# Kernel optimization log

Measured on AMD Instinct MI355X. Metric: run time of the kernel, lower is better.

The kernel has to match this reference:

```python
import jax, jax.numpy as jnp
import numpy as np

B, N, C, K, T = 64, 1024, 256, 512, 64
D_THRESH = 0.5
POWER_ITERS = 20


def _pdist(x):
    # x: [..., K, 3] -> pairwise euclidean distances [..., K, K]
    n = jnp.sum(x * x, axis=-1)
    sq = n[..., :, None] + n[..., None, :] - 2.0 * jnp.einsum('...kc,...lc->...kl', x, x)
    return jnp.sqrt(jnp.maximum(sq, 0.0) + 1e-12)


def _forward(rt, rt_centroids, rt_cls_attn, shift_and_scale, W_in, b_in, W1, b1, W2, b2,
             num_rt, anc_idx, pos_idx, neg_idx):
    valid = jnp.arange(N)[None, :] < num_rt[:, None]                      # [B,N]
    # Normalize.batch_unnormalize: pts * scale + shift on valid tokens
    shift = shift_and_scale[:, None, :3]
    scale = shift_and_scale[:, None, 3:4]
    cent = jnp.where(valid[..., None], rt_centroids * scale + shift, rt_centroids)
    attn = jnp.where(valid, rt_cls_attn, -1e9)
    _, top_idx = jax.lax.top_k(attn, K)                                   # [B,K]
    cent_k = jnp.take_along_axis(cent, top_idx[..., None], axis=1)        # [B,K,3]
    rt_k = jnp.take_along_axis(rt, top_idx[..., None], axis=1)            # [B,K,C]
    # SGV padding mask [T,2,K,K]: rows masked by anchor count, cols by pos/neg counts
    n_eff = jnp.minimum(num_rt, K)
    r = jnp.arange(K)
    row_mask = r[None, :] < n_eff[anc_idx][:, None]                       # [T,K]
    col_mask = jnp.stack([r[None, :] < n_eff[pos_idx][:, None],
                          r[None, :] < n_eff[neg_idx][:, None]], axis=1)  # [T,2,K]
    mask = row_mask[:, None, :, None] & col_mask[:, :, None, :]           # [T,2,K,K]
    # input_linear on anchor / neighbour relay tokens
    anc_f = rt_k[anc_idx] @ W_in + b_in                                   # [T,K,C]
    nn_f = jnp.stack([rt_k[pos_idx], rt_k[neg_idx]], axis=1) @ W_in + b_in  # [T,2,K,C]
    anc_c = cent_k[anc_idx]                                               # [T,K,3]
    nn_c = jnp.stack([cent_k[pos_idx], cent_k[neg_idx]], axis=1)          # [T,2,K,3]
    # feature-space nearest-neighbour correspondences anc -> nn (SpectralGV style)
    fd = (jnp.sum(anc_f ** 2, -1)[:, None, :, None]
          + jnp.sum(nn_f ** 2, -1)[:, :, None, :]
          - 2.0 * jnp.einsum('tkc,tnlc->tnkl', anc_f, nn_f))              # [T,2,K,K]
    corr = jnp.argmin(fd, axis=-1)                                        # [T,2,K]
    q_c = jnp.take_along_axis(nn_c, corr[..., None], axis=2)              # [T,2,K,3]
    q_f = jnp.take_along_axis(nn_f, corr[..., None], axis=2)              # [T,2,K,C]
    # correspondence confidence from feature cosine similarity
    cos = jnp.sum(anc_f[:, None] * q_f, -1) / (
        jnp.linalg.norm(anc_f, axis=-1)[:, None] * jnp.linalg.norm(q_f, axis=-1) + 1e-8)
    s = jax.nn.relu(cos)                                                  # [T,2,K]
    # threshold-masked geometric consistency adjacency
    d_p = _pdist(anc_c)[:, None]                                          # [T,1,K,K]
    d_q = _pdist(q_c)                                                     # [T,2,K,K]
    geo = (jnp.abs(d_p - d_q) < D_THRESH) & mask & (~jnp.eye(K, dtype=bool))
    A = geo.astype(jnp.float32) * s[..., :, None] * s[..., None, :]       # [T,2,K,K]
    # leading eigenvector via power iteration (A is entrywise nonnegative)
    v = jnp.full((T, 2, K), 1.0 / np.sqrt(K), dtype=jnp.float32)
    for _ in range(POWER_ITERS):
        w = jnp.einsum('tnkl,tnl->tnk', A, v)
        v = w / (jnp.linalg.norm(w, axis=-1, keepdims=True) + 1e-8)
    eig = -jnp.sort(-v, axis=-1)                                          # sort_eigvec, descending
    h = jax.nn.relu(eig @ W1 + b1)
    scores = jax.nn.sigmoid(h @ W2 + b2)                                  # [T,2,1]
    targets = jnp.zeros_like(scores).at[:, 0].set(1.0)
    return scores, targets


def setup_inputs() -> dict:
    key = jax.random.key(0)
    ks = jax.random.split(key, 12)
    return {
        'rt': jax.random.normal(ks[0], (B, N, C), jnp.float32),
        'rt_centroids': jax.random.normal(ks[1], (B, N, 3), jnp.float32),
        'rt_cls_attn': jax.random.uniform(ks[2], (B, N), jnp.float32),
        'shift_and_scale': jax.random.uniform(ks[3], (B, 4), jnp.float32),
        'num_rt': jax.random.randint(ks[4], (B,), 128, N, jnp.int32),
        'anc_idx': jax.random.randint(ks[5], (T,), 0, B, jnp.int32),
        'pos_idx': jax.random.randint(ks[6], (T,), 0, B, jnp.int32),
        'neg_idx': jax.random.randint(ks[7], (T,), 0, B, jnp.int32),
        'W_in': jax.random.normal(ks[8], (C, C), jnp.float32) / np.sqrt(C),
        'b_in': jnp.zeros((C,), jnp.float32),
        'W1': jax.random.normal(ks[9], (K, K), jnp.float32) / np.sqrt(K),
        'b1': jnp.zeros((K,), jnp.float32),
        'W2': jax.random.normal(ks[10], (K, 1), jnp.float32) / np.sqrt(K),
        'b2': jnp.zeros((1,), jnp.float32),
    }


def reference(rt, rt_centroids, rt_cls_attn, shift_and_scale, num_rt, anc_idx, pos_idx, neg_idx,
              W_in, b_in, W1, b1, W2, b2):
    return _forward(rt, rt_centroids, rt_cls_attn, shift_and_scale, W_in, b_in, W1, b1, W2, b2,
                    num_rt, anc_idx, pos_idx, neg_idx)
```

## Files before the change

### kernel.cpp

```cpp
#include <hip/hip_runtime.h>
#include <cstddef>

#define BB 64
#define NN 1024
#define CC 256
#define KK 512
#define TT 64
#define NPAIR 128

typedef _Float16 h8 __attribute__((ext_vector_type(8)));
typedef _Float16 h4 __attribute__((ext_vector_type(4)));
typedef float f4 __attribute__((ext_vector_type(4)));

typedef __attribute__((address_space(1))) const void GV;
typedef __attribute__((address_space(3))) void LV;
#define GLDS16(g, s) __builtin_amdgcn_global_load_lds((GV*)(const void*)(g), (LV*)(void*)(s), 16, 0, 0)


__global__ __launch_bounds__(256) void wtrans_kernel(
    const float* __restrict__ Win, _Float16* __restrict__ wth, _Float16* __restrict__ wtl)
{
    __shared__ float t[64][65];
    const int k0 = blockIdx.x * 64, n0 = blockIdx.y * 64;
    const int tid = threadIdx.x;
    const int c = tid & 63, r0 = tid >> 6;
    for (int r = r0; r < 64; r += 4)
        t[r][c] = Win[(size_t)(k0 + r) * CC + n0 + c];
    __syncthreads();
    for (int r = r0; r < 64; r += 4) {
        float x = t[c][r];
        _Float16 h = (_Float16)x;
        size_t o = (size_t)(n0 + r) * CC + k0 + c;
        wth[o] = h;
        wtl[o] = (_Float16)(x - (float)h);
    }
}

__global__ __launch_bounds__(512) void sel_kernel(
    const float* __restrict__ attn, const float* __restrict__ cents,
    const float* __restrict__ sas, const int* __restrict__ num_rt,
    int* __restrict__ topidx, int* __restrict__ neff, float* __restrict__ centk)
{
    __shared__ unsigned long long keys[1024];
    const int b = blockIdx.x, tid = threadIdx.x;
    const int nr = num_rt[b];
    for (int i = tid; i < 1024; i += 512) {
        float a = (i < nr) ? attn[b * NN + i] : -1e9f;
        unsigned u = __float_as_uint(a);
        u = (u & 0x80000000u) ? ~u : (u | 0x80000000u);
        keys[i] = ((unsigned long long)u << 32) | (unsigned)(0xFFFFFFFFu - (unsigned)i);
    }
    __syncthreads();
    for (int k = 2; k <= 1024; k <<= 1) {
        for (int j = k >> 1; j > 0; j >>= 1) {
            int i = ((tid & ~(j - 1)) << 1) | (tid & (j - 1));
            int p = i | j;
            unsigned long long a = keys[i], c = keys[p];
            bool up = (i & k) == 0;
            if (up ? (a < c) : (a > c)) { keys[i] = c; keys[p] = a; }
            __syncthreads();
        }
    }
    {
        unsigned long long key = keys[tid];
        int idx = (int)(~(unsigned)key);
        float x = cents[(b * NN + idx) * 3 + 0];
        float y = cents[(b * NN + idx) * 3 + 1];
        float z = cents[(b * NN + idx) * 3 + 2];
        if (idx < nr) {
            float sc = sas[b * 4 + 3];
            x = x * sc + sas[b * 4 + 0];
            y = y * sc + sas[b * 4 + 1];
            z = z * sc + sas[b * 4 + 2];
        }
        float nc = x * x + y * y + z * z;
        ((float4*)centk)[b * KK + tid] = make_float4(x, y, z, nc);
        topidx[b * KK + tid] = idx;
    }
    if (tid == 0) neff[b] = (nr < KK) ? nr : KK;
}

__global__ __launch_bounds__(256) void feat_mfma(
    const float* __restrict__ rt, const int* __restrict__ topidx,
    const _Float16* __restrict__ wth, const _Float16* __restrict__ wtl,
    const float* __restrict__ bin,
    _Float16* __restrict__ feath, _Float16* __restrict__ featl)
{
    const int mtile = blockIdx.x, nt = blockIdx.y;
    __shared__ _Float16 Ah[128][32], Al[128][32], Bh[128][32], Bl[128][32];
    __shared__ int tix[128];
    const int tid = threadIdx.x;
    const int w = tid >> 6, lane = tid & 63;
    const int quad = lane >> 4, l16 = lane & 15;
    const int wm = (w >> 1) * 64, wl = (w & 1) * 64;
    const int b = mtile >> 2;
    if (tid < 128) tix[tid] = topidx[mtile * 128 + tid];
    __syncthreads();
    const float* arow = (tid < 128) ? rt + ((size_t)b * NN + tix[tid]) * CC : rt;
    const _Float16* bplane = (w == 2) ? wth : wtl;
    _Float16* bsh = (w == 2) ? &Bh[0][0] : &Bl[0][0];
    const int rowi = lane >> 2, chunk = lane & 3;

    f4 acc[4][4];
    #pragma unroll
    for (int i = 0; i < 4; i++)
        #pragma unroll
        for (int j = 0; j < 4; j++)
            acc[i][j] = (f4){0.f, 0.f, 0.f, 0.f};

    for (int k0 = 0; k0 < CC; k0 += 32) {
        __syncthreads();
        if (w < 2) {
            const float4* src = (const float4*)(arow + k0);
            #pragma unroll
            for (int c = 0; c < 4; c++) {
                float4 p = src[2 * c], q2 = src[2 * c + 1];
                float xv[8] = {p.x, p.y, p.z, p.w, q2.x, q2.y, q2.z, q2.w};
                h8 hv, lv;
                #pragma unroll
                for (int j = 0; j < 8; j++) {
                    _Float16 h = (_Float16)xv[j];
                    hv[j] = h;
                    lv[j] = (_Float16)(xv[j] - (float)h);
                }
                *(h8*)&Ah[tid][c * 8] = hv;
                *(h8*)&Al[tid][c * 8] = lv;
            }
        } else {
            #pragma unroll
            for (int j = 0; j < 8; j++) {
                int row = j * 16 + rowi;
                const _Float16* ga = bplane + (size_t)(nt * 128 + row) * CC + k0 + chunk * 8;
                GLDS16(ga, bsh + j * 512);
            }
        }
        __syncthreads();
        h8 afh[4], afl[4], bfh[4], bfl[4];
        #pragma unroll
        for (int i = 0; i < 4; i++) {
            int ra = wm + i * 16 + l16;
            int rb = wl + i * 16 + l16;
            afh[i] = *(const h8*)&Ah[ra][quad * 8];
            afl[i] = *(const h8*)&Al[ra][quad * 8];
            bfh[i] = *(const h8*)&Bh[rb][quad * 8];
            bfl[i] = *(const h8*)&Bl[rb][quad * 8];
        }
        #pragma unroll
        for (int i = 0; i < 4; i++)
            #pragma unroll
            for (int j = 0; j < 4; j++) {
                acc[i][j] = __builtin_amdgcn_mfma_f32_16x16x32_f16(afh[i], bfh[j], acc[i][j], 0, 0, 0);
                acc[i][j] = __builtin_amdgcn_mfma_f32_16x16x32_f16(afh[i], bfl[j], acc[i][j], 0, 0, 0);
                acc[i][j] = __builtin_amdgcn_mfma_f32_16x16x32_f16(afl[i], bfh[j], acc[i][j], 0, 0, 0);
            }
    }
    #pragma unroll
    for (int j = 0; j < 4; j++) {
        int col = wl + j * 16 + l16;
        float bj = bin[nt * 128 + col];
        #pragma unroll
        for (int i = 0; i < 4; i++)
            #pragma unroll
            for (int r = 0; r < 4; r++) {
                int row = wm + i * 16 + quad * 4 + r;
                float v = acc[i][j][r] + bj;
                _Float16 h = (_Float16)v;
                size_t o = (size_t)(mtile * 128 + row) * CC + nt * 128 + col;
                feath[o] = h;
                featl[o] = (_Float16)(v - (float)h);
            }
    }
}

__global__ __launch_bounds__(256) void norm_kernel(
    const _Float16* __restrict__ feath, const _Float16* __restrict__ featl,
    float* __restrict__ normF)
{
    int r = blockIdx.x * 4 + (threadIdx.x >> 6);
    int lane = threadIdx.x & 63;
    h4 hv = ((const h4*)(feath + (size_t)r * CC))[lane];
    h4 lv = ((const h4*)(featl + (size_t)r * CC))[lane];
    float s = 0.f;
    #pragma unroll
    for (int j = 0; j < 4; j++) {
        float x = (float)hv[j] + (float)lv[j];
        s += x * x;
    }
    for (int off = 32; off; off >>= 1) s += __shfl_down(s, off);
    if (lane == 0) normF[r] = s;
}

__global__ __launch_bounds__(256) void argmin_mfma(
    const _Float16* __restrict__ feath, const _Float16* __restrict__ featl,
    const float* __restrict__ normF,
    const int* __restrict__ anc, const int* __restrict__ pos, const int* __restrict__ neg,
    float* __restrict__ partv, int* __restrict__ partl, float* __restrict__ partd)
{
    const int lt = blockIdx.x, kt = blockIdx.y, pr = blockIdx.z;
    const int t = pr >> 1, nn2 = pr & 1;
    const int a = anc[t];
    const int bb = nn2 ? neg[t] : pos[t];
    const size_t Abase = ((size_t)a * KK + kt * 128) * CC;
    const size_t Bbase = ((size_t)bb * KK + lt * 128) * CC;
    __shared__ _Float16 Ah[128][32], Al[128][32], Bh[128][32], Bl[128][32];
    __shared__ float rdv[128][2];
    __shared__ int   rdl[128][2];
    __shared__ float rdd[128][2];
    const int tid = threadIdx.x;
    const int w = tid >> 6, lane = tid & 63;
    const int quad = lane >> 4, l16 = lane & 15;
    const int wm = (w >> 1) * 64, wl = (w & 1) * 64;
    const int rowi = lane >> 2, chunk = lane & 3;
    const _Float16* gplane = (w == 0) ? feath + Abase : (w == 1) ? featl + Abase
                           : (w == 2) ? feath + Bbase : featl + Bbase;
    _Float16* splane = (w == 0) ? &Ah[0][0] : (w == 1) ? &Al[0][0]
                     : (w == 2) ? &Bh[0][0] : &Bl[0][0];
    const _Float16* grow = gplane + (size_t)rowi * CC + chunk * 8;

    f4 acc[4][4];
    #pragma unroll
    for (int i = 0; i < 4; i++)
        #pragma unroll
        for (int j = 0; j < 4; j++)
            acc[i][j] = (f4){0.f, 0.f, 0.f, 0.f};

    for (int k0 = 0; k0 < CC; k0 += 32) {
        __syncthreads();
        #pragma unroll
        for (int j = 0; j < 8; j++)
            GLDS16(grow + (size_t)(j * 16) * CC + k0, splane + j * 512);
        __syncthreads();
        h8 afh[4], afl[4], bfh[4], bfl[4];
        #pragma unroll
        for (int i = 0; i < 4; i++) {
            int ra = wm + i * 16 + l16;
            int rb = wl + i * 16 + l16;
            afh[i] = *(const h8*)&Ah[ra][quad * 8];
            afl[i] = *(const h8*)&Al[ra][quad * 8];
            bfh[i] = *(const h8*)&Bh[rb][quad * 8];
            bfl[i] = *(const h8*)&Bl[rb][quad * 8];
        }
        #pragma unroll
        for (int i = 0; i < 4; i++)
            #pragma unroll
            for (int j = 0; j < 4; j++) {
                acc[i][j] = __builtin_amdgcn_mfma_f32_16x16x32_f16(afh[i], bfh[j], acc[i][j], 0, 0, 0);
                acc[i][j] = __builtin_amdgcn_mfma_f32_16x16x32_f16(afh[i], bfl[j], acc[i][j], 0, 0, 0);
                acc[i][j] = __builtin_amdgcn_mfma_f32_16x16x32_f16(afl[i], bfh[j], acc[i][j], 0, 0, 0);
            }
    }
    float nbj[4];
    #pragma unroll
    for (int j = 0; j < 4; j++)
        nbj[j] = normF[(size_t)bb * KK + lt * 128 + wl + j * 16 + l16];
    #pragma unroll
    for (int i = 0; i < 4; i++) {
        #pragma unroll
        for (int r = 0; r < 4; r++) {
            float bv = INFINITY; int bl = 0; float bd = 0.f;
            #pragma unroll
            for (int j = 0; j < 4; j++) {
                float d = acc[i][j][r];
                float v = nbj[j] - 2.f * d;
                int l = lt * 128 + wl + j * 16 + l16;
                if (v < bv) { bv = v; bl = l; bd = d; }
            }
            #pragma unroll
            for (int off = 1; off < 16; off <<= 1) {
                float ov = __shfl_xor(bv, off);
                int   ol = __shfl_xor(bl, off);
                float od = __shfl_xor(bd, off);
                if (ov < bv || (ov == bv && ol < bl)) { bv = ov; bl = ol; bd = od; }
            }
            if (l16 == 0) {
                int row = wm + i * 16 + quad * 4 + r;
                rdv[row][w & 1] = bv;
                rdl[row][w & 1] = bl;
                rdd[row][w & 1] = bd;
            }
        }
    }
    __syncthreads();
    if (tid < 128) {
        float bv = rdv[tid][0]; int bl = rdl[tid][0]; float bd = rdd[tid][0];
        float v1 = rdv[tid][1]; int l1 = rdl[tid][1];
        if (v1 < bv || (v1 == bv && l1 < bl)) { bv = v1; bl = l1; bd = rdd[tid][1]; }
        size_t idx = (((size_t)pr * 4 + kt) * 128 + tid) * 4 + lt;
        partv[idx] = bv; partl[idx] = bl; partd[idx] = bd;
    }
}

__global__ __launch_bounds__(256) void argmin_fin(
    const float* __restrict__ partv, const int* __restrict__ partl,
    const float* __restrict__ partd, const float* __restrict__ normF,
    const int* __restrict__ anc, const int* __restrict__ pos, const int* __restrict__ neg,
    int* __restrict__ corr, float* __restrict__ sbuf)
{
    int g = blockIdx.x * 256 + threadIdx.x;
    int pr = g >> 9, kg = g & 511;
    int t = pr >> 1, nn2 = pr & 1;
    int a = anc[t];
    int bb = nn2 ? neg[t] : pos[t];
    size_t base = (size_t)g * 4;
    float bv = partv[base]; int bl = partl[base]; float bd = partd[base];
    #pragma unroll
    for (int lt = 1; lt < 4; lt++) {
        float v = partv[base + lt]; int l = partl[base + lt];
        if (v < bv || (v == bv && l < bl)) { bv = v; bl = l; bd = partd[base + lt]; }
    }
    float na = normF[(size_t)a * KK + kg];
    float nb = normF[(size_t)bb * KK + bl];
    float cosv = bd / (sqrtf(na) * sqrtf(nb) + 1e-8f);
    corr[g] = bl;
    sbuf[g] = fmaxf(cosv, 0.f);
}

__global__ __launch_bounds__(256) void geo_kernel(
    const float* __restrict__ centk, const int* __restrict__ corr,
    const int* __restrict__ neff,
    const int* __restrict__ anc, const int* __restrict__ pos, const int* __restrict__ neg,
    unsigned* __restrict__ gmask)
{
    const int kt = blockIdx.x;
    const int lt = blockIdx.y;
    const int pair = blockIdx.z;
    const int t = pair >> 1, nn2 = pair & 1;
    const int a = anc[t];
    const int bb2 = (nn2 == 0) ? pos[t] : neg[t];
    const int nea = neff[a], neb = neff[bb2];
    __shared__ __align__(16) float4 ca[512], cq[512];
    for (int i = threadIdx.x; i < KK; i += 256) {
        ca[i] = ((const float4*)centk)[a * KK + i];
        int c = corr[pair * KK + i];
        cq[i] = ((const float4*)centk)[bb2 * KK + c];
    }
    __syncthreads();
    const int k = kt * 256 + threadIdx.x;
    float4 pk = ca[k], qk = cq[k];
    bool rowm = k < nea;
    unsigned* outp = gmask + ((size_t)pair * KK + k) * 16 + lt * 4;
    for (int w = 0; w < 4; w++) {
        unsigned word = 0;
        #pragma unroll
        for (int bi = 0; bi < 32; bi++) {
            int l = lt * 128 + w * 32 + bi;
            float4 pl = ca[l], ql = cq[l];
            float dp2 = pk.w + pl.w - 2.f * (pk.x * pl.x + pk.y * pl.y + pk.z * pl.z);
            float dp = sqrtf(fmaxf(dp2, 0.f) + 1e-12f);
            float dq2 = qk.w + ql.w - 2.f * (qk.x * ql.x + qk.y * ql.y + qk.z * ql.z);
            float dq = sqrtf(fmaxf(dq2, 0.f) + 1e-12f);
            bool g = (fabsf(dp - dq) < 0.5f) && rowm && (l < neb) && (l != k);
            word |= (g ? (1u << bi) : 0u);
        }
        outp[w] = word;
    }
}

__global__ __launch_bounds__(1024, 4) void power_kernel(
    const unsigned* __restrict__ gmask, const float* __restrict__ sbuf,
    const float* __restrict__ W1, const float* __restrict__ b1,
    const float* __restrict__ W2, const float* __restrict__ b2,
    float* __restrict__ out)
{
    const int pair = blockIdx.x;
    const int tid = threadIdx.x;
    const int row = tid & 511;
    const int half = tid >> 9;
    __shared__ __align__(16) float u[512];
    __shared__ float T[64][257];
    __shared__ float pacc[1024];
    __shared__ float red[16];
    __shared__ float ev[512];
    __shared__ float hpart[1024];
    unsigned m[8];
    const unsigned* g = gmask + ((size_t)pair * KK + row) * 16 + half * 8;
    #pragma unroll
    for (int w = 0; w < 8; w++) m[w] = g[w];
    const float s = sbuf[pair * KK + row];
    const int bp = tid & 63;
    const int vh = tid >> 6;
    const int GV_[16] = {0,1,3,2,6,7,5,4,12,13,15,14,10,11,9,8};
    const int GB[15] = {0,1,0,2,0,1,0,3,0,1,0,2,0,1,0};
    const float GS[15] = {1.f,1.f,-1.f,1.f,1.f,-1.f,-1.f,1.f,1.f,1.f,-1.f,-1.f,1.f,-1.f,-1.f};
    float v = 0.044194173824159216f;
    if (half == 0) u[row] = s * v;
    __syncthreads();
    for (int it = 0; it < 20; it++) {
        {
            float4 ulo = *(const float4*)&u[bp * 8];
            float4 uhi = *(const float4*)&u[bp * 8 + 4];
            float ul[4] = {ulo.x, ulo.y, ulo.z, ulo.w};
            float H = 0.f;
            H += (float)((vh >> 0) & 1) * uhi.x;
            H += (float)((vh >> 1) & 1) * uhi.y;
            H += (float)((vh >> 2) & 1) * uhi.z;
            H += (float)((vh >> 3) & 1) * uhi.w;
            float L = 0.f;
            T[bp][vh * 16 + 0] = H;
            #pragma unroll
            for (int k = 1; k < 16; k++) {
                L += GS[k - 1] * ul[GB[k - 1]];
                T[bp][vh * 16 + GV_[k]] = H + L;
            }
        }
        __syncthreads();
        float a0 = 0.f, a1 = 0.f, a2 = 0.f, a3 = 0.f;
        #pragma unroll
        for (int w = 0; w < 8; w++) {
            unsigned mw = m[w];
            const int p0 = half * 32 + w * 4;
            a0 += T[p0 + 0][mw & 255u];
            a1 += T[p0 + 1][(mw >> 8) & 255u];
            a2 += T[p0 + 2][(mw >> 16) & 255u];
            a3 += T[p0 + 3][mw >> 24];
        }
        pacc[tid] = (a0 + a1) + (a2 + a3);
        __syncthreads();
        float wk = s * (pacc[row] + pacc[row + 512]);
        float t2 = wk * wk;
        for (int off = 32; off; off >>= 1) t2 += __shfl_down(t2, off);
        if ((tid & 63) == 0) red[tid >> 6] = t2;
        __syncthreads();
        float tot = 0.f;
        #pragma unroll
        for (int x = 0; x < 16; x++) tot += red[x];
        tot *= 0.5f;
        v = wk / (sqrtf(tot) + 1e-8f);
        if (half == 0) u[row] = s * v;
        __syncthreads();
    }
    if (half == 0) ev[row] = v;
    __syncthreads();
    for (int kk = 2; kk <= 512; kk <<= 1) {
        for (int j = kk >> 1; j; j >>= 1) {
            if (tid < 256) {
                int i = ((tid & ~(j - 1)) << 1) | (tid & (j - 1));
                int p = i | j;
                float x = ev[i], y = ev[p];
                bool up = (i & kk) == 0;
                if (up ? (x < y) : (x > y)) { ev[i] = y; ev[p] = x; }
            }
            __syncthreads();
        }
    }
    const int cbase = half * 256;
    float h = (half == 0) ? b1[row] : 0.f;
    #pragma unroll 8
    for (int l = 0; l < 256; l++)
        h += ev[cbase + l] * W1[(size_t)(cbase + l) * KK + row];
    hpart[tid] = h;
    __syncthreads();
    float term = 0.f;
    if (half == 0) {
        float hv = fmaxf(hpart[row] + hpart[row + 512], 0.f);
        term = hv * W2[row];
    }
    for (int off = 32; off; off >>= 1) term += __shfl_down(term, off);
    if ((tid & 63) == 0) red[tid >> 6] = term;
    __syncthreads();
    if (tid == 0) {
        float sc = 0.f;
        #pragma unroll
        for (int x = 0; x < 16; x++) sc += red[x];
        sc += b2[0];
        out[pair] = 1.f / (1.f + expf(-sc));
        out[NPAIR + pair] = (pair & 1) ? 0.f : 1.f;
    }
}

extern "C" void kernel_launch(void* const* d_in, const int* in_sizes, int n_in,
                              void* d_out, int out_size, void* d_ws, size_t ws_size,
                              hipStream_t stream) {
    (void)in_sizes; (void)n_in; (void)out_size; (void)ws_size;
    const float* rt    = (const float*)d_in[0];
    const float* cents = (const float*)d_in[1];
    const float* attn  = (const float*)d_in[2];
    const float* sas   = (const float*)d_in[3];
    const int* num_rt  = (const int*)d_in[4];
    const int* anc     = (const int*)d_in[5];
    const int* pos     = (const int*)d_in[6];
    const int* neg     = (const int*)d_in[7];
    const float* Win   = (const float*)d_in[8];
    const float* bin   = (const float*)d_in[9];
    const float* W1    = (const float*)d_in[10];
    const float* b1    = (const float*)d_in[11];
    const float* W2    = (const float*)d_in[12];
    const float* b2    = (const float*)d_in[13];

    float* ws = (float*)d_ws;
    _Float16* feath = (_Float16*)ws;
    _Float16* featl = (_Float16*)(ws + 4194304);
    float* normF = ws + 8388608;
    float* centk = ws + 8421376;
    float* sbuf  = ws + 8552448;
    int* topidx  = (int*)(ws + 8617984);
    int* neffp   = (int*)(ws + 8650752);
    int* corr    = (int*)(ws + 8650816);
    unsigned* gmask = (unsigned*)(ws + 8716352);
    float* partv = (float*)(ws + 8716352);
    int*   partl = (int*)(ws + 8716352 + 262144);
    float* partd = (float*)(ws + 8716352 + 524288);
    _Float16* wth = (_Float16*)(ws + 8716352 + 786432);
    _Float16* wtl = (_Float16*)(ws + 8716352 + 819200);
    float* out = (float*)d_out;

    wtrans_kernel<<<dim3(4, 4), 256, 0, stream>>>(Win, wth, wtl);
    sel_kernel<<<64, 512, 0, stream>>>(attn, cents, sas, num_rt, topidx, neffp, centk);
    feat_mfma<<<dim3(256, 2), 256, 0, stream>>>(rt, topidx, wth, wtl, bin, feath, featl);
    norm_kernel<<<8192, 256, 0, stream>>>(feath, featl, normF);
    argmin_mfma<<<dim3(4, 4, 128), 256, 0, stream>>>(feath, featl, normF, anc, pos, neg, partv, partl, partd);
    argmin_fin<<<256, 256, 0, stream>>>(partv, partl, partd, normF, anc, pos, neg, corr, sbuf);
    geo_kernel<<<dim3(2, 4, 128), 256, 0, stream>>>(centk, corr, neffp, anc, pos, neg, gmask);
    power_kernel<<<128, 1024, 0, stream>>>(gmask, sbuf, W1, b1, W2, b2, out);
}
```

Before: 376.5 us.

## Share anchor tile across pos and neg pairs in argmin MFMA kernel

Each argmin block now handles both the positive and negative neighbour for a triplet, using 512 threads. The anchor hi/lo tiles are loaded into shared memory once and reused by both halves, so anchor global loads drop by about half and the grid shrinks from 2048 to 1024 blocks. In exchange each block uses more LDS and more threads, which may reduce occupancy, and two waves sit idle during loads.

```diff
diff --git a/kernel.cpp b/kernel.cpp
--- a/kernel.cpp
+++ b/kernel.cpp
@@ -190,32 +190,38 @@
     if (lane == 0) normF[r] = s;
 }
 
-__global__ __launch_bounds__(256) void argmin_mfma(
+__global__ __launch_bounds__(512) void argmin_mfma(
     const _Float16* __restrict__ feath, const _Float16* __restrict__ featl,
     const float* __restrict__ normF,
     const int* __restrict__ anc, const int* __restrict__ pos, const int* __restrict__ neg,
     float* __restrict__ partv, int* __restrict__ partl, float* __restrict__ partd)
 {
-    const int lt = blockIdx.x, kt = blockIdx.y, pr = blockIdx.z;
-    const int t = pr >> 1, nn2 = pr & 1;
-    const int a = anc[t];
-    const int bb = nn2 ? neg[t] : pos[t];
+    const int lt = blockIdx.x, kt = blockIdx.y, t = blockIdx.z;
+    const int a = anc[t], bp = pos[t], bn = neg[t];
     const size_t Abase = ((size_t)a * KK + kt * 128) * CC;
-    const size_t Bbase = ((size_t)bb * KK + lt * 128) * CC;
-    __shared__ _Float16 Ah[128][32], Al[128][32], Bh[128][32], Bl[128][32];
-    __shared__ float rdv[128][2];
-    __shared__ int   rdl[128][2];
-    __shared__ float rdd[128][2];
+    const size_t Pbase = ((size_t)bp * KK + lt * 128) * CC;
+    const size_t Nbase = ((size_t)bn * KK + lt * 128) * CC;
+    __shared__ _Float16 smem[6 * 4096];
+    __shared__ float rdv[2][128][2];
+    __shared__ int   rdl[2][128][2];
+    __shared__ float rdd[2][128][2];
     const int tid = threadIdx.x;
     const int w = tid >> 6, lane = tid & 63;
     const int quad = lane >> 4, l16 = lane & 15;
-    const int wm = (w >> 1) * 64, wl = (w & 1) * 64;
+    const int pair = w & 1, wmI = (w >> 1) & 1, wlI = (w >> 2) & 1;
+    const int wm = wmI * 64, wl = wlI * 64;
     const int rowi = lane >> 2, chunk = lane & 3;
-    const _Float16* gplane = (w == 0) ? feath + Abase : (w == 1) ? featl + Abase
-                           : (w == 2) ? feath + Bbase : featl + Bbase;
-    _Float16* splane = (w == 0) ? &Ah[0][0] : (w == 1) ? &Al[0][0]
-                     : (w == 2) ? &Bh[0][0] : &Bl[0][0];
+    const _Float16* gplane =
+        (w == 0) ? feath + Abase : (w == 1) ? featl + Abase :
+        (w == 2) ? feath + Pbase : (w == 3) ? featl + Pbase :
+        (w == 4) ? feath + Nbase : featl + Nbase;
+    _Float16* splane = smem + (w < 6 ? w : 0) * 4096;
     const _Float16* grow = gplane + (size_t)rowi * CC + chunk * 8;
+    const _Float16* Ah = smem;
+    const _Float16* Al = smem + 4096;
+    const _Float16* Bhp = smem + (pair ? 4 : 2) * 4096;
+    const _Float16* Blp = smem + (pair ? 5 : 3) * 4096;
+    const int bb = pair ? bn : bp;
 
     f4 acc[4][4];
     #pragma unroll
@@ -226,19 +232,21 @@
 
     for (int k0 = 0; k0 < CC; k0 += 32) {
         __syncthreads();
-        #pragma unroll
-        for (int j = 0; j < 8; j++)
-            GLDS16(grow + (size_t)(j * 16) * CC + k0, splane + j * 512);
+        if (w < 6) {
+            #pragma unroll
+            for (int j = 0; j < 8; j++)
+                GLDS16(grow + (size_t)(j * 16) * CC + k0, splane + j * 512);
+        }
         __syncthreads();
         h8 afh[4], afl[4], bfh[4], bfl[4];
         #pragma unroll
         for (int i = 0; i < 4; i++) {
             int ra = wm + i * 16 + l16;
             int rb = wl + i * 16 + l16;
-            afh[i] = *(const h8*)&Ah[ra][quad * 8];
-            afl[i] = *(const h8*)&Al[ra][quad * 8];
-            bfh[i] = *(const h8*)&Bh[rb][quad * 8];
-            bfl[i] = *(const h8*)&Bl[rb][quad * 8];
+            afh[i] = *(const h8*)&Ah[ra * 32 + quad * 8];
+            afl[i] = *(const h8*)&Al[ra * 32 + quad * 8];
+            bfh[i] = *(const h8*)&Bhp[rb * 32 + quad * 8];
+            bfl[i] = *(const h8*)&Blp[rb * 32 + quad * 8];
         }
         #pragma unroll
         for (int i = 0; i < 4; i++)
@@ -274,18 +282,20 @@
             }
             if (l16 == 0) {
                 int row = wm + i * 16 + quad * 4 + r;
-                rdv[row][w & 1] = bv;
-                rdl[row][w & 1] = bl;
-                rdd[row][w & 1] = bd;
-            }
-        }
-    }
-    __syncthreads();
-    if (tid < 128) {
-        float bv = rdv[tid][0]; int bl = rdl[tid][0]; float bd = rdd[tid][0];
-        float v1 = rdv[tid][1]; int l1 = rdl[tid][1];
-        if (v1 < bv || (v1 == bv && l1 < bl)) { bv = v1; bl = l1; bd = rdd[tid][1]; }
-        size_t idx = (((size_t)pr * 4 + kt) * 128 + tid) * 4 + lt;
+                rdv[pair][row][wlI] = bv;
+                rdl[pair][row][wlI] = bl;
+                rdd[pair][row][wlI] = bd;
+            }
+        }
+    }
+    __syncthreads();
+    if (tid < 256) {
+        const int pairIdx = tid >> 7, row = tid & 127;
+        float bv = rdv[pairIdx][row][0]; int bl = rdl[pairIdx][row][0]; float bd = rdd[pairIdx][row][0];
+        float v1 = rdv[pairIdx][row][1]; int l1 = rdl[pairIdx][row][1];
+        if (v1 < bv || (v1 == bv && l1 < bl)) { bv = v1; bl = l1; bd = rdd[pairIdx][row][1]; }
+        int pr = t * 2 + pairIdx;
+        size_t idx = (((size_t)pr * 4 + kt) * 128 + row) * 4 + lt;
         partv[idx] = bv; partl[idx] = bl; partd[idx] = bd;
     }
 }
@@ -508,7 +518,7 @@
     sel_kernel<<<64, 512, 0, stream>>>(attn, cents, sas, num_rt, topidx, neffp, centk);
     feat_mfma<<<dim3(256, 2), 256, 0, stream>>>(rt, topidx, wth, wtl, bin, feath, featl);
     norm_kernel<<<8192, 256, 0, stream>>>(feath, featl, normF);
-    argmin_mfma<<<dim3(4, 4, 128), 256, 0, stream>>>(feath, featl, normF, anc, pos, neg, partv, partl, partd);
+    argmin_mfma<<<dim3(4, 4, 64), 512, 0, stream>>>(feath, featl, normF, anc, pos, neg, partv, partl, partd);
     argmin_fin<<<256, 256, 0, stream>>>(partv, partl, partd, normF, anc, pos, neg, corr, sbuf);
     geo_kernel<<<dim3(2, 4, 128), 256, 0, stream>>>(centk, corr, neffp, anc, pos, neg, gmask);
     power_kernel<<<128, 1024, 0, stream>>>(gmask, sbuf, W1, b1, W2, b2, out);
```

Result: slower. 386.5 us (+2.7%).

## Fuse argmin finalization into geo kernel and rebalance feat_mfma load roles

Applied to the files above, without the earlier changes.

The separate argmin_fin launch is removed. Each geo_kernel block now reduces the four partial argmin candidates itself to get the correspondence indices, and only one block per pair writes the cosine scores. This saves a launch and the corr round trip through global memory, but every one of the 8 blocks per pair repeats the small reduction. Separately, feat_mfma now has all four waves share the A-row fp32-to-fp16 split (two threads per row) and the B-tile async LDS loads, instead of splitting waves between the two tasks. The partial buffers are moved so they no longer alias gmask, since both are now live in the same kernel.

```diff
diff --git a/kernel.cpp b/kernel.cpp
--- a/kernel.cpp
+++ b/kernel.cpp
@@ -96,9 +96,11 @@
     const int b = mtile >> 2;
     if (tid < 128) tix[tid] = topidx[mtile * 128 + tid];
     __syncthreads();
-    const float* arow = (tid < 128) ? rt + ((size_t)b * NN + tix[tid]) * CC : rt;
-    const _Float16* bplane = (w == 2) ? wth : wtl;
-    _Float16* bsh = (w == 2) ? &Bh[0][0] : &Bl[0][0];
+    const int arow_i = tid >> 1;
+    const int aseg = (tid & 1) * 16;
+    const float* arow = rt + ((size_t)b * NN + tix[arow_i]) * CC + aseg;
+    _Float16* bsh = (w < 2) ? &Bh[0][0] : &Bl[0][0];
+    const _Float16* bplane = (w < 2) ? wth : wtl;
     const int rowi = lane >> 2, chunk = lane & 3;
 
     f4 acc[4][4];
@@ -110,10 +112,16 @@
 
     for (int k0 = 0; k0 < CC; k0 += 32) {
         __syncthreads();
-        if (w < 2) {
+        #pragma unroll
+        for (int jj = 0; jj < 4; jj++) {
+            int j = (w & 1) * 4 + jj;
+            int row = j * 16 + rowi;
+            GLDS16(bplane + (size_t)(nt * 128 + row) * CC + k0 + chunk * 8, bsh + j * 512);
+        }
+        {
             const float4* src = (const float4*)(arow + k0);
             #pragma unroll
-            for (int c = 0; c < 4; c++) {
+            for (int c = 0; c < 2; c++) {
                 float4 p = src[2 * c], q2 = src[2 * c + 1];
                 float xv[8] = {p.x, p.y, p.z, p.w, q2.x, q2.y, q2.z, q2.w};
                 h8 hv, lv;
@@ -123,15 +131,8 @@
                     hv[j] = h;
                     lv[j] = (_Float16)(xv[j] - (float)h);
                 }
-                *(h8*)&Ah[tid][c * 8] = hv;
-                *(h8*)&Al[tid][c * 8] = lv;
-            }
-        } else {
-            #pragma unroll
-            for (int j = 0; j < 8; j++) {
-                int row = j * 16 + rowi;
-                const _Float16* ga = bplane + (size_t)(nt * 128 + row) * CC + k0 + chunk * 8;
-                GLDS16(ga, bsh + j * 512);
+                *(h8*)&Ah[arow_i][aseg + c * 8] = hv;
+                *(h8*)&Al[arow_i][aseg + c * 8] = lv;
             }
         }
         __syncthreads();
@@ -290,60 +291,55 @@
     }
 }
 
-__global__ __launch_bounds__(256) void argmin_fin(
+__global__ __launch_bounds__(256) void geo_kernel(
+    const float* __restrict__ centk,
     const float* __restrict__ partv, const int* __restrict__ partl,
     const float* __restrict__ partd, const float* __restrict__ normF,
-    const int* __restrict__ anc, const int* __restrict__ pos, const int* __restrict__ neg,
-    int* __restrict__ corr, float* __restrict__ sbuf)
-{
-    int g = blockIdx.x * 256 + threadIdx.x;
-    int pr = g >> 9, kg = g & 511;
-    int t = pr >> 1, nn2 = pr & 1;
-    int a = anc[t];
-    int bb = nn2 ? neg[t] : pos[t];
-    size_t base = (size_t)g * 4;
-    float bv = partv[base]; int bl = partl[base]; float bd = partd[base];
-    #pragma unroll
-    for (int lt = 1; lt < 4; lt++) {
-        float v = partv[base + lt]; int l = partl[base + lt];
-        if (v < bv || (v == bv && l < bl)) { bv = v; bl = l; bd = partd[base + lt]; }
-    }
-    float na = normF[(size_t)a * KK + kg];
-    float nb = normF[(size_t)bb * KK + bl];
-    float cosv = bd / (sqrtf(na) * sqrtf(nb) + 1e-8f);
-    corr[g] = bl;
-    sbuf[g] = fmaxf(cosv, 0.f);
-}
-
-__global__ __launch_bounds__(256) void geo_kernel(
-    const float* __restrict__ centk, const int* __restrict__ corr,
     const int* __restrict__ neff,
     const int* __restrict__ anc, const int* __restrict__ pos, const int* __restrict__ neg,
-    unsigned* __restrict__ gmask)
+    float* __restrict__ sbuf, unsigned* __restrict__ gmask)
 {
     const int kt = blockIdx.x;
-    const int lt = blockIdx.y;
+    const int lt4 = blockIdx.y;
     const int pair = blockIdx.z;
     const int t = pair >> 1, nn2 = pair & 1;
     const int a = anc[t];
     const int bb2 = (nn2 == 0) ? pos[t] : neg[t];
     const int nea = neff[a], neb = neff[bb2];
+    const bool writer = (kt == 0) && (lt4 == 0);
+    __shared__ int ci[512];
     __shared__ __align__(16) float4 ca[512], cq[512];
     for (int i = threadIdx.x; i < KK; i += 256) {
+        size_t base = ((size_t)pair * KK + i) * 4;
+        float bv = partv[base]; int bl = partl[base]; float bd = partd[base];
+        #pragma unroll
+        for (int lt = 1; lt < 4; lt++) {
+            float v = partv[base + lt]; int l = partl[base + lt];
+            if (v < bv || (v == bv && l < bl)) { bv = v; bl = l; bd = partd[base + lt]; }
+        }
+        ci[i] = bl;
+        if (writer) {
+            float na = normF[(size_t)a * KK + i];
+            float nb = normF[(size_t)bb2 * KK + bl];
+            float cosv = bd / (sqrtf(na) * sqrtf(nb) + 1e-8f);
+            sbuf[pair * KK + i] = fmaxf(cosv, 0.f);
+        }
+    }
+    __syncthreads();
+    for (int i = threadIdx.x; i < KK; i += 256) {
         ca[i] = ((const float4*)centk)[a * KK + i];
-        int c = corr[pair * KK + i];
-        cq[i] = ((const float4*)centk)[bb2 * KK + c];
+        cq[i] = ((const float4*)centk)[bb2 * KK + ci[i]];
     }
     __syncthreads();
     const int k = kt * 256 + threadIdx.x;
     float4 pk = ca[k], qk = cq[k];
     bool rowm = k < nea;
-    unsigned* outp = gmask + ((size_t)pair * KK + k) * 16 + lt * 4;
+    unsigned* outp = gmask + ((size_t)pair * KK + k) * 16 + lt4 * 4;
     for (int w = 0; w < 4; w++) {
         unsigned word = 0;
         #pragma unroll
         for (int bi = 0; bi < 32; bi++) {
-            int l = lt * 128 + w * 32 + bi;
+            int l = lt4 * 128 + w * 32 + bi;
             float4 pl = ca[l], ql = cq[l];
             float dp2 = pk.w + pl.w - 2.f * (pk.x * pl.x + pk.y * pl.y + pk.z * pl.z);
             float dp = sqrtf(fmaxf(dp2, 0.f) + 1e-12f);
@@ -495,13 +491,12 @@
     float* sbuf  = ws + 8552448;
     int* topidx  = (int*)(ws + 8617984);
     int* neffp   = (int*)(ws + 8650752);
-    int* corr    = (int*)(ws + 8650816);
     unsigned* gmask = (unsigned*)(ws + 8716352);
-    float* partv = (float*)(ws + 8716352);
-    int*   partl = (int*)(ws + 8716352 + 262144);
-    float* partd = (float*)(ws + 8716352 + 524288);
     _Float16* wth = (_Float16*)(ws + 8716352 + 786432);
     _Float16* wtl = (_Float16*)(ws + 8716352 + 819200);
+    float* partv = (float*)(ws + 9764928);
+    int*   partl = (int*)(ws + 10027072);
+    float* partd = (float*)(ws + 10289216);
     float* out = (float*)d_out;
 
     wtrans_kernel<<<dim3(4, 4), 256, 0, stream>>>(Win, wth, wtl);
@@ -509,7 +504,6 @@
     feat_mfma<<<dim3(256, 2), 256, 0, stream>>>(rt, topidx, wth, wtl, bin, feath, featl);
     norm_kernel<<<8192, 256, 0, stream>>>(feath, featl, normF);
     argmin_mfma<<<dim3(4, 4, 128), 256, 0, stream>>>(feath, featl, normF, anc, pos, neg, partv, partl, partd);
-    argmin_fin<<<256, 256, 0, stream>>>(partv, partl, partd, normF, anc, pos, neg, corr, sbuf);
-    geo_kernel<<<dim3(2, 4, 128), 256, 0, stream>>>(centk, corr, neffp, anc, pos, neg, gmask);
+    geo_kernel<<<dim3(2, 4, 128), 256, 0, stream>>>(centk, partv, partl, partd, normF, neffp, anc, pos, neg, sbuf, gmask);
     power_kernel<<<128, 1024, 0, stream>>>(gmask, sbuf, W1, b1, W2, b2, out);
 }
```

Measured after the change: 372.0 us. About the same (-1.2%).
